# Kernel optimization log

Measured on AMD Instinct MI355X. Metric: run time of the kernel, lower is better.

## Reference

```python
import jax, jax.numpy as jnp
import numpy as np

# Basis functions chosen for the instantiation:
#   f0 = sin(x)        (arity 1)
#   f1 = x * y         (arity 2, cartesian product over feature pairs)
#   f2 = identity      (auto-appended by the module)
# torch.cartesian_prod(a, a) enumerates pairs with the FIRST index varying
# slowest, which matches a row-major reshape of the [d, d] outer grid.

B, D = 256, 512


def setup_inputs() -> dict:
    key = jax.random.key(0)
    x = jax.random.normal(key, (B, D), dtype=jnp.float32)
    return {"x": x}


def reference(x):
    b, d = x.shape
    # arity-1: sin applied to every feature -> [B, d]
    sin_part = jnp.sin(x)
    # arity-2: product over the cartesian grid of features.
    # x[:, i, None] * x[:, None, j] -> [B, d, d]; row-major reshape matches
    # torch.cartesian_prod ordering (i slow, j fast). -> [B, d*d]
    pair_part = (x[:, :, None] * x[:, None, :]).reshape(b, d * d)
    # appended identity -> [B, d]
    ident_part = x
    # concat in function order: [sin, mul2, identity] -> [B, d + d^2 + d]
    return jnp.concatenate([sin_part, pair_part, ident_part], axis=1)
```

## Files before the change

### kernel.cpp

```cpp
#include <hip/hip_runtime.h>
#include <cmath>

constexpr int B = 256;
constexpr int D = 512;
constexpr int ROW = D + D * D + D;
constexpr int PAIR_ROWS_PER_BLOCK = 32;
constexpr int PAIR_BLOCKS = D / PAIR_ROWS_PER_BLOCK;
constexpr int BLOCKS_PER_BATCH = PAIR_BLOCKS + 1;

typedef float f4 __attribute__((ext_vector_type(4)));

__global__ __launch_bounds__(256)
void basis_expansion_kernel(const float* __restrict__ x, float* __restrict__ out) {
    const int bid  = blockIdx.x;
    const int b    = bid / BLOCKS_PER_BATCH;
    const int part = bid % BLOCKS_PER_BATCH;
    const int t    = threadIdx.x;

    const float* xrow = x + b * D;
    float* orow = out + (size_t)b * ROW;

    __shared__ float sx[D];
    sx[t]       = xrow[t];
    sx[t + 256] = xrow[t + 256];
    __syncthreads();

    const int col4 = t & 127;
    const f4 v = reinterpret_cast<const f4*>(sx)[col4];

    if (part == PAIR_BLOCKS) {
        if (t < 128) {
            f4 s;
            s.x = sinf(v.x); s.y = sinf(v.y); s.z = sinf(v.z); s.w = sinf(v.w);
            __builtin_nontemporal_store(s, reinterpret_cast<f4*>(orow) + col4);
        } else {
            __builtin_nontemporal_store(v, reinterpret_cast<f4*>(orow + D + D * D) + col4);
        }
        return;
    }

    const int row0 = part * PAIR_ROWS_PER_BLOCK + (t >> 7);
    f4* pbase = reinterpret_cast<f4*>(orow + D);

#pragma unroll
    for (int m = 0; m < PAIR_ROWS_PER_BLOCK / 2; ++m) {
        const int row = row0 + 2 * m;
        const float a = sx[row];
        f4 w;
        w.x = a * v.x; w.y = a * v.y; w.z = a * v.z; w.w = a * v.w;
        __builtin_nontemporal_store(w, pbase + (row * 128 + col4));
    }
}

extern "C" void kernel_launch(void* const* d_in, const int* in_sizes, int n_in,
                              void* d_out, int out_size, void* d_ws, size_t ws_size,
                              hipStream_t stream) {
    const float* x = (const float*)d_in[0];
    float* out = (float*)d_out;
    dim3 grid(B * BLOCKS_PER_BATCH);
    dim3 block(256);
    basis_expansion_kernel<<<grid, block, 0, stream>>>(x, out);
}
```

Before: 265.2 us.

## Switch to persistent grid-stride kernel reading x directly from global

Replaces the per-batch block decomposition (17 blocks per batch row, using shared memory staging) with a fixed grid of 2048 blocks that grid-stride over 2-row chunks of the pair output. The x loads now come straight from global/L2 instead of shared memory, and the sin and identity segments are handled by the first 64 blocks after the pair loop. The aim is to cut block launch and scheduling overhead and the __syncthreads, so the kernel behaves more like a steady streaming store. In exchange, x is re-read from cache on every iteration and the extra tail work is unevenly spread across blocks.

```diff
diff --git a/kernel.cpp b/kernel.cpp
--- a/kernel.cpp
+++ b/kernel.cpp
@@ -4,51 +4,56 @@
 constexpr int B = 256;
 constexpr int D = 512;
 constexpr int ROW = D + D * D + D;
-constexpr int PAIR_ROWS_PER_BLOCK = 32;
-constexpr int PAIR_BLOCKS = D / PAIR_ROWS_PER_BLOCK;
-constexpr int BLOCKS_PER_BATCH = PAIR_BLOCKS + 1;
+constexpr int G = 2048;
+constexpr int CHUNKS = B * 256;
+constexpr int ITERS = CHUNKS / G;
 
 typedef float f4 __attribute__((ext_vector_type(4)));
 
 __global__ __launch_bounds__(256)
 void basis_expansion_kernel(const float* __restrict__ x, float* __restrict__ out) {
     const int bid  = blockIdx.x;
-    const int b    = bid / BLOCKS_PER_BATCH;
-    const int part = bid % BLOCKS_PER_BATCH;
     const int t    = threadIdx.x;
+    const int half = t >> 7;
+    const int col4 = t & 127;
 
-    const float* xrow = x + b * D;
-    float* orow = out + (size_t)b * ROW;
+    const f4* x4 = reinterpret_cast<const f4*>(x);
 
-    __shared__ float sx[D];
-    sx[t]       = xrow[t];
-    sx[t + 256] = xrow[t + 256];
-    __syncthreads();
-
-    const int col4 = t & 127;
-    const f4 v = reinterpret_cast<const f4*>(sx)[col4];
-
-    if (part == PAIR_BLOCKS) {
-        if (t < 128) {
-            f4 s;
-            s.x = sinf(v.x); s.y = sinf(v.y); s.z = sinf(v.z); s.w = sinf(v.w);
-            __builtin_nontemporal_store(s, reinterpret_cast<f4*>(orow) + col4);
-        } else {
-            __builtin_nontemporal_store(v, reinterpret_cast<f4*>(orow + D + D * D) + col4);
-        }
-        return;
+#pragma unroll 4
+    for (int k = 0; k < ITERS; ++k) {
+        const int c   = k * G + bid;
+        const int b   = c >> 8;
+        const int ci  = c & 255;
+        const int row = ci * 2 + half;
+        const float a = x[b * D + row];
+        const f4 v = x4[b * 128 + col4];
+        f4 w;
+        w.x = a * v.x; w.y = a * v.y; w.z = a * v.z; w.w = a * v.w;
+        f4* dst = reinterpret_cast<f4*>(out + (size_t)b * ROW + D) + (row * 128 + col4);
+        __builtin_nontemporal_store(w, dst);
     }
 
-    const int row0 = part * PAIR_ROWS_PER_BLOCK + (t >> 7);
-    f4* pbase = reinterpret_cast<f4*>(orow + D);
-
+    if (bid < 64) {
+        const int s = bid * 256 + t;
 #pragma unroll
-    for (int m = 0; m < PAIR_ROWS_PER_BLOCK / 2; ++m) {
-        const int row = row0 + 2 * m;
-        const float a = sx[row];
-        f4 w;
-        w.x = a * v.x; w.y = a * v.y; w.z = a * v.z; w.w = a * v.w;
-        __builtin_nontemporal_store(w, pbase + (row * 128 + col4));
+        for (int q0 = 0; q0 < 4; ++q0) {
+            const int q = q0 * 16384 + s;
+            const int b = q >> 8;
+            const int r = q & 255;
+            const f4* xr = x4 + b * 128;
+            float* orow = out + (size_t)b * ROW;
+            if (r < 128) {
+                const f4 vv = xr[r];
+                f4 sres;
+                sres.x = sinf(vv.x); sres.y = sinf(vv.y);
+                sres.z = sinf(vv.z); sres.w = sinf(vv.w);
+                __builtin_nontemporal_store(sres, reinterpret_cast<f4*>(orow) + r);
+            } else {
+                const f4 vv = xr[r - 128];
+                __builtin_nontemporal_store(vv,
+                    reinterpret_cast<f4*>(orow + D + D * D) + (r - 128));
+            }
+        }
     }
 }
 
@@ -57,7 +62,7 @@
                               hipStream_t stream) {
     const float* x = (const float*)d_in[0];
     float* out = (float*)d_out;
-    dim3 grid(B * BLOCKS_PER_BATCH);
+    dim3 grid(G);
     dim3 block(256);
     basis_expansion_kernel<<<grid, block, 0, stream>>>(x, out);
 }
```

Measured after the change: 271.9 us. +2.5%, slower.
